# Kernel optimization log

Hardware: AMD Instinct MI355X
Metric: run time of the kernel (lower is better)

Reference implementation:

```python
import jax, jax.numpy as jnp
import numpy as np

B, DX, DZ, DY = 8192, 512, 1024, 256


def setup_inputs() -> dict:
    key = jax.random.key(0)
    ks = jax.random.split(key, 13)
    s = 0.02
    return {
        "xs": jax.random.normal(ks[0], (B, DX), dtype=jnp.float32),
        "Wx": jax.random.normal(ks[1], (DZ, DX), dtype=jnp.float32) * s,
        "bx": jnp.zeros((DZ,), dtype=jnp.float32),
        "Wy": jax.random.normal(ks[2], (DZ, DY), dtype=jnp.float32) * s,
        "by": jnp.zeros((DZ,), dtype=jnp.float32),
        "Wn": jax.random.normal(ks[3], (DZ, 3 * DZ), dtype=jnp.float32) * s,
        "bn": jnp.zeros((DZ,), dtype=jnp.float32),
        "Wu": jax.random.normal(ks[4], (DY, DZ), dtype=jnp.float32) * s,
        "bu": jnp.zeros((DY,), dtype=jnp.float32),
        "Wq": jax.random.normal(ks[5], (DY, DZ), dtype=jnp.float32) * s,
        "bq": jnp.zeros((DY,), dtype=jnp.float32),
        "ys_init": jax.random.normal(ks[6], (B, DY), dtype=jnp.float32),
        "zs_init": jax.random.normal(ks[7], (B, DZ), dtype=jnp.float32),
        "T": 4,
        "n": 6,
    }


def reference(xs, Wx, bx, Wy, by, Wn, bn, Wu, bu, Wq, bq, ys_init, zs_init, T, n):
    xs_e = xs @ Wx.T + bx                      # [B, DZ]
    ys_e = ys_init @ Wy.T + by                 # [B, DZ]
    zs = zs_init                               # [B, DZ]
    null = jnp.zeros_like(xs_e)

    def query(x, y, z):
        w = jnp.concatenate([x, y, z], axis=-1)  # [B, 3*DZ]
        return jnp.tanh(w @ Wn.T + bn)

    # no-grad refinement (T-1 outer iterations)
    for _ in range(T - 1):
        for _ in range(n):
            zs = query(xs_e, ys_e, zs)
        ys_e = query(null, ys_e, zs)
    ys_e = jax.lax.stop_gradient(ys_e)
    zs = jax.lax.stop_gradient(zs)

    # final grad-enabled block
    for _ in range(n):
        zs = query(xs_e, ys_e, zs)
    ys_e = query(null, ys_e, zs)

    y_hat = jax.nn.sigmoid(ys_e @ Wu.T + bu)
    q_hat = jax.nn.sigmoid(ys_e @ Wq.T + bq)
    return (y_hat, q_hat)
```

## Files before the change

### kernel.cpp

```cpp
#include <hip/hip_runtime.h>
#include <hip/hip_bf16.h>
#include <cstdint>
#include <cstddef>

#define B_   8192
#define DX_  512
#define DZ_  1024
#define DY_  256
#define T_   4
#define NN_  6

typedef float f32x4 __attribute__((ext_vector_type(4)));
typedef short s16x8 __attribute__((ext_vector_type(8)));
typedef long i64x2 __attribute__((ext_vector_type(2)));
typedef __hip_bfloat16 bf16;

__device__ __forceinline__ void gload_lds16(const void* g, void* l) {
  __builtin_amdgcn_global_load_lds(
      (const __attribute__((address_space(1))) void*)g,
      (__attribute__((address_space(3))) void*)l,
      16, 0, 0);
}

__device__ __forceinline__ float bf2f(unsigned short u) {
  union { unsigned int i; float f; } cv; cv.i = ((unsigned int)u) << 16; return cv.f;
}

__device__ __forceinline__ int permb(int n) {
  return (n & ~63) | (((n >> 3) & 3) << 4) | (((n >> 5) & 1) << 3) | (n & 7);
}

__device__ __forceinline__ void cv4(const float* __restrict__ s, bf16* __restrict__ d, long i) {
  float4 v = ((const float4*)s)[i];
  ushort4 o;
  bf16 a0 = __float2bfloat16(v.x); o.x = *(unsigned short*)&a0;
  bf16 a1 = __float2bfloat16(v.y); o.y = *(unsigned short*)&a1;
  bf16 a2 = __float2bfloat16(v.z); o.z = *(unsigned short*)&a2;
  bf16 a3 = __float2bfloat16(v.w); o.w = *(unsigned short*)&a3;
  ((ushort4*)d)[i] = o;
}
__device__ __forceinline__ void cv4f8(const float* __restrict__ src, unsigned char* __restrict__ dst,
                                      long row, int k0, int srcld, int srcoff) {
  float4 v = *(const float4*)(src + row * srcld + srcoff + k0);
  int p = __builtin_amdgcn_cvt_pk_fp8_f32(v.x, v.y, 0, 0);
  p = __builtin_amdgcn_cvt_pk_fp8_f32(v.z, v.w, p, 1);
  *(int*)(dst + row * DZ_ + permb(k0)) = p;
}

__global__ void cvt_all_kernel(const float* __restrict__ Wn, const float* __restrict__ Wx,
                               const float* __restrict__ Wy, const float* __restrict__ Wu,
                               const float* __restrict__ Wq, const float* __restrict__ xs,
                               const float* __restrict__ ys0, const float* __restrict__ zs0,
                               const float* __restrict__ bu, const float* __restrict__ bq,
                               bf16* __restrict__ Wn_b, bf16* __restrict__ Wx_b,
                               bf16* __restrict__ Wy_b, bf16* __restrict__ Wuq_b,
                               bf16* __restrict__ xs_b, bf16* __restrict__ ysin_b,
                               float* __restrict__ buq,
                               unsigned char* __restrict__ Wnz8, unsigned char* __restrict__ z_a8) {
  const long NWN = (long)DZ_ * 3 * DZ_ / 4, NWX = (long)DZ_ * DX_ / 4,
             NWY = (long)DZ_ * DY_ / 4,     NWU = (long)DY_ * DZ_ / 4,
             NXS = (long)B_ * DX_ / 4,      NYS = (long)B_ * DY_ / 4,
             NBQ = 2 * DY_ / 4,
             NW8 = (long)DZ_ * DZ_ / 4,     NZ8 = (long)B_ * DZ_ / 4;
  const long total = NWN + NWX + NWY + 2 * NWU + NXS + NYS + NBQ + NW8 + NZ8;
  for (long i = (long)blockIdx.x * blockDim.x + threadIdx.x; i < total;
       i += (long)gridDim.x * blockDim.x) {
    long j = i;
    if (j < NWN) { cv4(Wn, Wn_b, j); continue; } j -= NWN;
    if (j < NWX) { cv4(Wx, Wx_b, j); continue; } j -= NWX;
    if (j < NWY) { cv4(Wy, Wy_b, j); continue; } j -= NWY;
    if (j < NWU) { cv4(Wu, Wuq_b, j); continue; } j -= NWU;
    if (j < NWU) { cv4(Wq, Wuq_b + (size_t)DY_ * DZ_, j); continue; } j -= NWU;
    if (j < NXS) { cv4(xs, xs_b, j); continue; } j -= NXS;
    if (j < NYS) { cv4(ys0, ysin_b, j); continue; } j -= NYS;
    if (j < NBQ) {
      float4 v = (j < DY_ / 4) ? ((const float4*)bu)[j] : ((const float4*)bq)[j - DY_ / 4];
      ((float4*)buq)[j] = v; continue;
    } j -= NBQ;
    if (j < NW8) {
      long e = j * 4; long row = e >> 10; int k0 = (int)(e & 1023);
      cv4f8(Wn, Wnz8, row, k0, 3 * DZ_, 2 * DZ_); continue;
    } j -= NW8;
    {
      long e = j * 4; long row = e >> 10; int k0 = (int)(e & 1023);
      cv4f8(zs0, z_a8, row, k0, DZ_, 0);
    }
  }
}

template<int ACT, int MODE, bool HASADD>
__global__ __launch_bounds__(512, 2)
void gemm_bt(const bf16* __restrict__ A, int lda,
             const bf16* __restrict__ W, int ldw,
             const float* __restrict__ bias,
             const bf16* __restrict__ add1,
             bf16* __restrict__ out_pre,
             void* __restrict__ out, void* __restrict__ out2,
             int N, int K)
{
  __shared__ __align__(16) char ldsc[4 * 24576];
  const int t    = threadIdx.x;
  const int lane = t & 63;
  const int wave = t >> 6;
  const int m0 = blockIdx.x * 256;
  const int n0 = blockIdx.y * 128;

  const int srow = t >> 2;
  const int q    = (t & 3) ^ ((t >> 3) & 3);
  const bf16* gA = A + (size_t)(m0 + srow) * lda + q * 8;
  const bf16* gB = W + (size_t)(n0 + srow) * ldw + q * 8;
  const int wb = wave * 1024;

  auto stage = [&](int kt) {
    char* base = ldsc + (kt & 3) * 24576;
    const int ko = kt << 5;
    gload_lds16(gA + ko, base + wb);
    gload_lds16(gA + (size_t)128 * lda + ko, base + 8192 + wb);
    gload_lds16(gB + ko, base + 16384 + wb);
  };

  const int mo = (wave >> 1) * 64;
  const int no = (wave & 1) * 64;
  const int fr = lane & 15;
  const int g4 = lane >> 4;
  const int rb = g4 * 4;
  const int cb = (g4 ^ ((fr >> 1) & 3)) * 16;

  const int NT = K >> 5;

  float bv[4] = {0.f, 0.f, 0.f, 0.f};
  if (bias) {
#pragma unroll
    for (int j = 0; j < 4; ++j) bv[j] = bias[n0 + no + j * 16 + fr];
  }
  unsigned short adr[4][4][4];
  if (HASADD && MODE != 1) {
#pragma unroll
    for (int f = 0; f < 4; ++f)
#pragma unroll
      for (int j = 0; j < 4; ++j) {
        const unsigned short* p = (const unsigned short*)add1
            + (size_t)(m0 + mo + f * 16 + rb) * N + (n0 + no + j * 16 + fr);
#pragma unroll
        for (int r = 0; r < 4; ++r) adr[f][j][r] = p[(size_t)r * N];
      }
  }
  __builtin_amdgcn_sched_barrier(0);
  stage(0); stage(1); stage(2);
  __builtin_amdgcn_sched_barrier(0);

  f32x4 acc[4][4];
#pragma unroll
  for (int f = 0; f < 4; ++f)
#pragma unroll
    for (int j = 0; j < 4; ++j)
#pragma unroll
      for (int r = 0; r < 4; ++r) {
        float v = bv[j];
        if (HASADD && MODE != 1) v += bf2f(adr[f][j][r]);
        acc[f][j][r] = v;
      }

  asm volatile("s_waitcnt vmcnt(6)" ::: "memory");
  __builtin_amdgcn_s_barrier();
  __builtin_amdgcn_sched_barrier(0);

  for (int kt = 0; kt < NT; ++kt) {
    const char* pA = ldsc + (kt & 3) * 24576;
    const char* pB = pA + 16384;
    s16x8 fa[4], fb[4];
#pragma unroll
    for (int f = 0; f < 4; ++f) fa[f] = *(const s16x8*)(pA + (mo + f * 16 + fr) * 64 + cb);
#pragma unroll
    for (int j = 0; j < 4; ++j) fb[j] = *(const s16x8*)(pB + (no + j * 16 + fr) * 64 + cb);
    if (kt + 3 < NT) stage(kt + 3);
    __builtin_amdgcn_sched_barrier(0);
    asm volatile("s_waitcnt lgkmcnt(0)" ::: "memory");
    __builtin_amdgcn_sched_barrier(0);
    __builtin_amdgcn_s_setprio(1);
#pragma unroll
    for (int f = 0; f < 4; ++f)
#pragma unroll
      for (int j = 0; j < 4; ++j)
        acc[f][j] = __builtin_amdgcn_mfma_f32_16x16x32_bf16(fa[f], fb[j], acc[f][j], 0, 0, 0);
    __builtin_amdgcn_s_setprio(0);
    const int rem = NT - 1 - kt;
    if (rem >= 3)      asm volatile("s_waitcnt vmcnt(6)" ::: "memory");
    else if (rem == 2) asm volatile("s_waitcnt vmcnt(3)" ::: "memory");
    else if (rem == 1) asm volatile("s_waitcnt vmcnt(0)" ::: "memory");
    if (rem >= 1) {
      __builtin_amdgcn_s_barrier();
      __builtin_amdgcn_sched_barrier(0);
    }
  }

#pragma unroll
  for (int f = 0; f < 4; ++f) {
#pragma unroll
    for (int j = 0; j < 4; ++j) {
      const int n = n0 + no + j * 16 + fr;
#pragma unroll
      for (int r = 0; r < 4; ++r) {
        const int m = m0 + mo + f * 16 + rb + r;
        float v = acc[f][j][r];
        if (MODE == 1) {
          out_pre[(size_t)m * N + n] = __float2bfloat16(v);
          v += bf2f(((const unsigned short*)add1)[(size_t)m * N + n]);
        }
        if (ACT == 1)      { float e = __expf(2.f * v); v = 1.f - 2.f / (e + 1.f); }
        else if (ACT == 2) v = 1.f / (1.f + __expf(-v));
        if (MODE == 2) {
          if (n < DY_) ((float*)out)[(size_t)m * DY_ + n] = v;
          else         ((float*)out2)[(size_t)m * DY_ + (n - DY_)] = v;
        } else {
          ((bf16*)out)[(size_t)m * N + n] = __float2bfloat16(v);
        }
      }
    }
  }
}

__global__ __launch_bounds__(512, 2)
void gemm_f8(const unsigned char* __restrict__ A8,
             const unsigned char* __restrict__ W8,
             const bf16* __restrict__ add1,
             unsigned char* __restrict__ out8,
             bf16* __restrict__ out16)
{
  __shared__ __align__(16) char ldsc[4 * 24576];
  const int t    = threadIdx.x;
  const int lane = t & 63;
  const int wave = t >> 6;
  const int m0 = blockIdx.x * 256;
  const int n0 = blockIdx.y * 128;

  const int srow = t >> 2;
  const int q    = (t & 3) ^ ((t >> 3) & 3);
  const unsigned char* gA = A8 + (size_t)(m0 + srow) * DZ_ + q * 16;
  const unsigned char* gB = W8 + (size_t)(n0 + srow) * DZ_ + q * 16;
  const int wb = wave * 1024;

  auto stage = [&](int kt) {
    char* base = ldsc + (kt & 3) * 24576;
    const int ko = kt << 6;
    gload_lds16(gA + ko, base + wb);
    gload_lds16(gA + (size_t)128 * DZ_ + ko, base + 8192 + wb);
    gload_lds16(gB + ko, base + 16384 + wb);
  };

  const int mo = (wave >> 1) * 64;
  const int no = (wave & 1) * 64;
  const int fr = lane & 15;
  const int g4 = lane >> 4;
  const int rb = g4 * 4;
  const int cb = (g4 ^ ((fr >> 1) & 3)) * 16;

  const int NT = DZ_ >> 6;

  unsigned short adr[4][4][4];
#pragma unroll
  for (int f = 0; f < 4; ++f)
#pragma unroll
    for (int j = 0; j < 4; ++j) {
      const unsigned short* p = (const unsigned short*)add1
          + (size_t)(m0 + mo + f * 16 + rb) * DZ_ + (n0 + no + j * 16 + fr);
#pragma unroll
      for (int r = 0; r < 4; ++r) adr[f][j][r] = p[(size_t)r * DZ_];
    }
  __builtin_amdgcn_sched_barrier(0);
  stage(0); stage(1); stage(2);
  __builtin_amdgcn_sched_barrier(0);

  f32x4 acc[4][4];
#pragma unroll
  for (int f = 0; f < 4; ++f)
#pragma unroll
    for (int j = 0; j < 4; ++j)
#pragma unroll
      for (int r = 0; r < 4; ++r) acc[f][j][r] = bf2f(adr[f][j][r]);

  asm volatile("s_waitcnt vmcnt(6)" ::: "memory");
  __builtin_amdgcn_s_barrier();
  __builtin_amdgcn_sched_barrier(0);

  for (int kt = 0; kt < NT; ++kt) {
    const char* pA = ldsc + (kt & 3) * 24576;
    const char* pB = pA + 16384;
    i64x2 av[4], bv[4];
#pragma unroll
    for (int f = 0; f < 4; ++f) av[f] = *(const i64x2*)(pA + (mo + f * 16 + fr) * 64 + cb);
#pragma unroll
    for (int j = 0; j < 4; ++j) bv[j] = *(const i64x2*)(pB + (no + j * 16 + fr) * 64 + cb);
    if (kt + 3 < NT) stage(kt + 3);
    __builtin_amdgcn_sched_barrier(0);
    asm volatile("s_waitcnt lgkmcnt(0)" ::: "memory");
    __builtin_amdgcn_sched_barrier(0);
    __builtin_amdgcn_s_setprio(1);
#pragma unroll
    for (int f = 0; f < 4; ++f)
#pragma unroll
      for (int j = 0; j < 4; ++j) {
        acc[f][j] = __builtin_amdgcn_mfma_f32_16x16x32_fp8_fp8(av[f][0], bv[j][0], acc[f][j], 0, 0, 0);
        acc[f][j] = __builtin_amdgcn_mfma_f32_16x16x32_fp8_fp8(av[f][1], bv[j][1], acc[f][j], 0, 0, 0);
      }
    __builtin_amdgcn_s_setprio(0);
    const int rem = NT - 1 - kt;
    if (rem >= 3)      asm volatile("s_waitcnt vmcnt(6)" ::: "memory");
    else if (rem == 2) asm volatile("s_waitcnt vmcnt(3)" ::: "memory");
    else if (rem == 1) asm volatile("s_waitcnt vmcnt(0)" ::: "memory");
    if (rem >= 1) {
      __builtin_amdgcn_s_barrier();
      __builtin_amdgcn_sched_barrier(0);
    }
  }

#pragma unroll
  for (int f = 0; f < 4; ++f) {
#pragma unroll
    for (int j = 0; j < 4; ++j) {
      const int n = n0 + no + j * 16 + fr;
      const int np = permb(n);
#pragma unroll
      for (int r = 0; r < 4; ++r) {
        const int m = m0 + mo + f * 16 + rb + r;
        float v = acc[f][j][r];
        float e = __expf(2.f * v); v = 1.f - 2.f / (e + 1.f);
        if (out8)  out8[(size_t)m * DZ_ + np] =
            (unsigned char)__builtin_amdgcn_cvt_pk_fp8_f32(v, v, 0, 0);
        if (out16) out16[(size_t)m * DZ_ + n] = __float2bfloat16(v);
      }
    }
  }
}

extern "C" void kernel_launch(void* const* d_in, const int* in_sizes, int n_in,
                              void* d_out, int out_size, void* d_ws, size_t ws_size,
                              hipStream_t stream) {
  const float* xs  = (const float*)d_in[0];
  const float* Wx  = (const float*)d_in[1];
  const float* bx  = (const float*)d_in[2];
  const float* Wy  = (const float*)d_in[3];
  const float* by  = (const float*)d_in[4];
  const float* Wn  = (const float*)d_in[5];
  const float* bn  = (const float*)d_in[6];
  const float* Wu  = (const float*)d_in[7];
  const float* bu  = (const float*)d_in[8];
  const float* Wq  = (const float*)d_in[9];
  const float* bq  = (const float*)d_in[10];
  const float* ys0 = (const float*)d_in[11];
  const float* zs0 = (const float*)d_in[12];

  char* ws = (char*)d_ws;
  size_t off = 0;
  auto take = [&](size_t bytes) -> char* {
    char* p = ws + off;
    off += (bytes + 255) & ~(size_t)255;
    return p;
  };

  bf16*  Wn_b   = (bf16*)take((size_t)DZ_ * 3 * DZ_ * 2);
  bf16*  Wx_b   = (bf16*)take((size_t)DZ_ * DX_ * 2);
  bf16*  Wy_b   = (bf16*)take((size_t)DZ_ * DY_ * 2);
  bf16*  Wuq_b  = (bf16*)take((size_t)2 * DY_ * DZ_ * 2);
  float* buq    = (float*)take((size_t)2 * DY_ * 4);
  bf16*  ys_b   = (bf16*)take((size_t)B_ * DZ_ * 2);
  bf16*  z_a    = (bf16*)take((size_t)B_ * DZ_ * 2);
  bf16*  z_b    = (bf16*)take((size_t)B_ * DZ_ * 2);
  bf16*  cx     = (bf16*)take((size_t)B_ * DZ_ * 2);
  bf16*  cy     = (bf16*)take((size_t)B_ * DZ_ * 2);
  bf16*  c      = (bf16*)take((size_t)B_ * DZ_ * 2);
  unsigned char* Wnz8 = (unsigned char*)take((size_t)DZ_ * DZ_);
  unsigned char* z_a8 = (unsigned char*)take((size_t)B_ * DZ_);
  unsigned char* z_b8 = (unsigned char*)take((size_t)B_ * DZ_);
  bf16* xs_b   = c;
  bf16* ysin_b = (bf16*)((char*)c + (size_t)B_ * DX_ * 2);
  bf16* xse_b  = cy;

  cvt_all_kernel<<<2048, 256, 0, stream>>>(Wn, Wx, Wy, Wu, Wq, xs, ys0, zs0, bu, bq,
                                           Wn_b, Wx_b, Wy_b, Wuq_b,
                                           xs_b, ysin_b, buq, Wnz8, z_a8);

  const dim3 blk(512);
  const dim3 gz(B_ / 256, DZ_ / 128);
  const dim3 gh(B_ / 256, 4);

  gemm_bt<0, 0, false><<<gz, blk, 0, stream>>>(xs_b, DX_, Wx_b, DX_, bx, nullptr, nullptr, xse_b, nullptr, DZ_, DX_);
  gemm_bt<0, 0, false><<<gz, blk, 0, stream>>>(ysin_b, DY_, Wy_b, DY_, by, nullptr, nullptr, ys_b, nullptr, DZ_, DY_);
  gemm_bt<0, 0, false><<<gz, blk, 0, stream>>>(xse_b, DZ_, Wn_b, 3 * DZ_, nullptr, nullptr, nullptr, cx, nullptr, DZ_, DZ_);

  unsigned char* zc8 = z_a8;
  unsigned char* zn8 = z_b8;
  for (int tt = 0; tt < T_; ++tt) {
    gemm_bt<0, 1, true><<<gz, blk, 0, stream>>>(ys_b, DZ_, Wn_b + DZ_, 3 * DZ_, bn, cx, cy, c, nullptr, DZ_, DZ_);
    if (tt < T_ - 1) {
      for (int i = 0; i < NN_; ++i) {
        bf16* shadow = (tt == T_ - 2 && i == NN_ - 1) ? z_a : nullptr;
        gemm_f8<<<gz, blk, 0, stream>>>(zc8, Wnz8, c, zn8, shadow);
        unsigned char* t8 = zc8; zc8 = zn8; zn8 = t8;
      }
      gemm_f8<<<gz, blk, 0, stream>>>(zc8, Wnz8, cy, nullptr, ys_b);
    } else {
      bf16* zc = z_a;
      bf16* zn = z_b;
      for (int i = 0; i < NN_; ++i) {
        gemm_bt<1, 0, true><<<gz, blk, 0, stream>>>(zc, DZ_, Wn_b + 2 * DZ_, 3 * DZ_, nullptr, c, nullptr, zn, nullptr, DZ_, DZ_);
        bf16* tmp = zc; zc = zn; zn = tmp;
      }
      gemm_bt<1, 0, true><<<gz, blk, 0, stream>>>(zc, DZ_, Wn_b + 2 * DZ_, 3 * DZ_, nullptr, cy, nullptr, ys_b, nullptr, DZ_, DZ_);
    }
  }

  float* outp = (float*)d_out;
  gemm_bt<2, 2, false><<<gh, blk, 0, stream>>>(ys_b, DZ_, Wuq_b, DZ_, buq, nullptr, nullptr,
                                               outp, outp + (size_t)B_ * DY_, 2 * DY_, DZ_);
}
```

Before: 829.8 us.

## Switch fp8 z-recurrence GEMM to 16x16x128 scaled MFMA with 128-wide K tiles

```diff
diff --git a/kernel.cpp b/kernel.cpp
--- a/kernel.cpp
+++ b/kernel.cpp
@@ -12,7 +12,8 @@
 
 typedef float f32x4 __attribute__((ext_vector_type(4)));
 typedef short s16x8 __attribute__((ext_vector_type(8)));
-typedef long i64x2 __attribute__((ext_vector_type(2)));
+typedef int   i32x4 __attribute__((ext_vector_type(4)));
+typedef int   i32x8 __attribute__((ext_vector_type(8)));
 typedef __hip_bfloat16 bf16;
 
 __device__ __forceinline__ void gload_lds16(const void* g, void* l) {
@@ -24,10 +25,6 @@
 
 __device__ __forceinline__ float bf2f(unsigned short u) {
   union { unsigned int i; float f; } cv; cv.i = ((unsigned int)u) << 16; return cv.f;
-}
-
-__device__ __forceinline__ int permb(int n) {
-  return (n & ~63) | (((n >> 3) & 3) << 4) | (((n >> 5) & 1) << 3) | (n & 7);
 }
 
 __device__ __forceinline__ void cv4(const float* __restrict__ s, bf16* __restrict__ d, long i) {
@@ -44,7 +41,7 @@
   float4 v = *(const float4*)(src + row * srcld + srcoff + k0);
   int p = __builtin_amdgcn_cvt_pk_fp8_f32(v.x, v.y, 0, 0);
   p = __builtin_amdgcn_cvt_pk_fp8_f32(v.z, v.w, p, 1);
-  *(int*)(dst + row * DZ_ + permb(k0)) = p;
+  *(int*)(dst + row * DZ_ + k0) = p;
 }
 
 __global__ void cvt_all_kernel(const float* __restrict__ Wn, const float* __restrict__ Wx,
@@ -220,32 +217,35 @@
   }
 }
 
-__global__ __launch_bounds__(512, 2)
-void gemm_f8(const unsigned char* __restrict__ A8,
-             const unsigned char* __restrict__ W8,
-             const bf16* __restrict__ add1,
-             unsigned char* __restrict__ out8,
-             bf16* __restrict__ out16)
+__global__ __launch_bounds__(512, 1)
+void gemm_f8mx(const unsigned char* __restrict__ A8,
+               const unsigned char* __restrict__ W8,
+               const bf16* __restrict__ add1,
+               unsigned char* __restrict__ out8,
+               bf16* __restrict__ out16)
 {
-  __shared__ __align__(16) char ldsc[4 * 24576];
+  __shared__ __align__(16) char ldsc[3 * 49152];
   const int t    = threadIdx.x;
   const int lane = t & 63;
   const int wave = t >> 6;
   const int m0 = blockIdx.x * 256;
   const int n0 = blockIdx.y * 128;
 
-  const int srow = t >> 2;
-  const int q    = (t & 3) ^ ((t >> 3) & 3);
-  const unsigned char* gA = A8 + (size_t)(m0 + srow) * DZ_ + q * 16;
-  const unsigned char* gB = W8 + (size_t)(n0 + srow) * DZ_ + q * 16;
+  const int srow = t >> 3;
+  const int q8   = (t & 7) ^ ((t >> 3) & 7);
+  const unsigned char* gA = A8 + (size_t)(m0 + srow) * DZ_ + q8 * 16;
+  const unsigned char* gB = W8 + (size_t)(n0 + srow) * DZ_ + q8 * 16;
   const int wb = wave * 1024;
 
   auto stage = [&](int kt) {
-    char* base = ldsc + (kt & 3) * 24576;
-    const int ko = kt << 6;
-    gload_lds16(gA + ko, base + wb);
-    gload_lds16(gA + (size_t)128 * DZ_ + ko, base + 8192 + wb);
-    gload_lds16(gB + ko, base + 16384 + wb);
+    char* base = ldsc + (kt % 3) * 49152;
+    const int ko = kt << 7;
+#pragma unroll
+    for (int i = 0; i < 4; ++i)
+      gload_lds16(gA + (size_t)(i * 64) * DZ_ + ko, base + i * 8192 + wb);
+#pragma unroll
+    for (int i = 0; i < 2; ++i)
+      gload_lds16(gB + (size_t)(i * 64) * DZ_ + ko, base + 32768 + i * 8192 + wb);
   };
 
   const int mo = (wave >> 1) * 64;
@@ -253,9 +253,10 @@
   const int fr = lane & 15;
   const int g4 = lane >> 4;
   const int rb = g4 * 4;
-  const int cb = (g4 ^ ((fr >> 1) & 3)) * 16;
-
-  const int NT = DZ_ >> 6;
+  const int p0 = (((g4 << 1) ^ (fr & 7)) << 4);
+  const int p1 = p0 ^ 16;
+
+  const int NT = DZ_ >> 7;
 
   unsigned short adr[4][4][4];
 #pragma unroll
@@ -268,7 +269,7 @@
       for (int r = 0; r < 4; ++r) adr[f][j][r] = p[(size_t)r * DZ_];
     }
   __builtin_amdgcn_sched_barrier(0);
-  stage(0); stage(1); stage(2);
+  stage(0); stage(1);
   __builtin_amdgcn_sched_barrier(0);
 
   f32x4 acc[4][4];
@@ -284,14 +285,26 @@
   __builtin_amdgcn_sched_barrier(0);
 
   for (int kt = 0; kt < NT; ++kt) {
-    const char* pA = ldsc + (kt & 3) * 24576;
-    const char* pB = pA + 16384;
-    i64x2 av[4], bv[4];
-#pragma unroll
-    for (int f = 0; f < 4; ++f) av[f] = *(const i64x2*)(pA + (mo + f * 16 + fr) * 64 + cb);
-#pragma unroll
-    for (int j = 0; j < 4; ++j) bv[j] = *(const i64x2*)(pB + (no + j * 16 + fr) * 64 + cb);
-    if (kt + 3 < NT) stage(kt + 3);
+    const char* pA = ldsc + (kt % 3) * 49152;
+    const char* pB = pA + 32768;
+    i32x8 av[4], bv[4];
+#pragma unroll
+    for (int f = 0; f < 4; ++f) {
+      const char* rp = pA + (mo + f * 16 + fr) * 128;
+      i32x4 lo = *(const i32x4*)(rp + p0);
+      i32x4 hi = *(const i32x4*)(rp + p1);
+      av[f][0] = lo[0]; av[f][1] = lo[1]; av[f][2] = lo[2]; av[f][3] = lo[3];
+      av[f][4] = hi[0]; av[f][5] = hi[1]; av[f][6] = hi[2]; av[f][7] = hi[3];
+    }
+#pragma unroll
+    for (int j = 0; j < 4; ++j) {
+      const char* rp = pB + (no + j * 16 + fr) * 128;
+      i32x4 lo = *(const i32x4*)(rp + p0);
+      i32x4 hi = *(const i32x4*)(rp + p1);
+      bv[j][0] = lo[0]; bv[j][1] = lo[1]; bv[j][2] = lo[2]; bv[j][3] = lo[3];
+      bv[j][4] = hi[0]; bv[j][5] = hi[1]; bv[j][6] = hi[2]; bv[j][7] = hi[3];
+    }
+    if (kt + 2 < NT) stage(kt + 2);
     __builtin_amdgcn_sched_barrier(0);
     asm volatile("s_waitcnt lgkmcnt(0)" ::: "memory");
     __builtin_amdgcn_sched_barrier(0);
@@ -299,16 +312,13 @@
 #pragma unroll
     for (int f = 0; f < 4; ++f)
 #pragma unroll
-      for (int j = 0; j < 4; ++j) {
-        acc[f][j] = __builtin_amdgcn_mfma_f32_16x16x32_fp8_fp8(av[f][0], bv[j][0], acc[f][j], 0, 0, 0);
-        acc[f][j] = __builtin_amdgcn_mfma_f32_16x16x32_fp8_fp8(av[f][1], bv[j][1], acc[f][j], 0, 0, 0);
-      }
+      for (int j = 0; j < 4; ++j)
+        acc[f][j] = __builtin_amdgcn_mfma_scale_f32_16x16x128_f8f6f4(
+            av[f], bv[j], acc[f][j], 0, 0, 0, 0x7f7f7f7f, 0, 0x7f7f7f7f);
     __builtin_amdgcn_s_setprio(0);
-    const int rem = NT - 1 - kt;
-    if (rem >= 3)      asm volatile("s_waitcnt vmcnt(6)" ::: "memory");
-    else if (rem == 2) asm volatile("s_waitcnt vmcnt(3)" ::: "memory");
-    else if (rem == 1) asm volatile("s_waitcnt vmcnt(0)" ::: "memory");
-    if (rem >= 1) {
+    if (kt + 2 < NT)      asm volatile("s_waitcnt vmcnt(6)" ::: "memory");
+    else if (kt + 1 < NT) asm volatile("s_waitcnt vmcnt(0)" ::: "memory");
+    if (kt + 1 < NT) {
       __builtin_amdgcn_s_barrier();
       __builtin_amdgcn_sched_barrier(0);
     }
@@ -319,13 +329,12 @@
 #pragma unroll
     for (int j = 0; j < 4; ++j) {
       const int n = n0 + no + j * 16 + fr;
-      const int np = permb(n);
 #pragma unroll
       for (int r = 0; r < 4; ++r) {
         const int m = m0 + mo + f * 16 + rb + r;
         float v = acc[f][j][r];
         float e = __expf(2.f * v); v = 1.f - 2.f / (e + 1.f);
-        if (out8)  out8[(size_t)m * DZ_ + np] =
+        if (out8)  out8[(size_t)m * DZ_ + n] =
             (unsigned char)__builtin_amdgcn_cvt_pk_fp8_f32(v, v, 0, 0);
         if (out16) out16[(size_t)m * DZ_ + n] = __float2bfloat16(v);
       }
@@ -395,10 +404,10 @@
     if (tt < T_ - 1) {
       for (int i = 0; i < NN_; ++i) {
         bf16* shadow = (tt == T_ - 2 && i == NN_ - 1) ? z_a : nullptr;
-        gemm_f8<<<gz, blk, 0, stream>>>(zc8, Wnz8, c, zn8, shadow);
+        gemm_f8mx<<<gz, blk, 0, stream>>>(zc8, Wnz8, c, zn8, shadow);
         unsigned char* t8 = zc8; zc8 = zn8; zn8 = t8;
       }
-      gemm_f8<<<gz, blk, 0, stream>>>(zc8, Wnz8, cy, nullptr, ys_b);
+      gemm_f8mx<<<gz, blk, 0, stream>>>(zc8, Wnz8, cy, nullptr, ys_b);
     } else {
       bf16* zc = z_a;
       bf16* zn = z_b;
```

Result: slower. 3.259 ms (+292.7%).
